# Optimization experiments

Hardware: AMD Instinct MI355X
Metric: run time of the kernel (lower is better)

Reference implementation:

```python
import jax, jax.numpy as jnp
import numpy as np

B, S, D, H, FF = 4, 2048, 1024, 16, 4096
HD = D // H


def setup_inputs() -> dict:
    key = jax.random.key(0)
    ks = jax.random.split(key, 12)
    s = 1.0 / np.sqrt(D)
    sf = 1.0 / np.sqrt(FF)
    return {
        "x": jax.random.normal(ks[0], (B, S, D), dtype=jnp.float32),
        "lengths": jax.random.randint(ks[1], (B,), 1, S + 1, dtype=jnp.int32),
        "qW": jax.random.uniform(ks[2], (D, D), jnp.float32, -s, s),
        "qb": jnp.zeros((D,), jnp.float32),
        "kW": jax.random.uniform(ks[3], (D, D), jnp.float32, -s, s),
        "kb": jnp.zeros((D,), jnp.float32),
        "vW": jax.random.uniform(ks[4], (D, D), jnp.float32, -s, s),
        "vb": jnp.zeros((D,), jnp.float32),
        "oW": jax.random.uniform(ks[5], (D, D), jnp.float32, -s, s),
        "ob": jnp.zeros((D,), jnp.float32),
        "w1": jax.random.uniform(ks[6], (D, FF), jnp.float32, -s, s),
        "b1": jnp.zeros((FF,), jnp.float32),
        "w2": jax.random.uniform(ks[7], (FF, D), jnp.float32, -sf, sf),
        "b2": jnp.zeros((D,), jnp.float32),
    }


def _heads(t):
    # [B,S,D] -> [B,H,S,HD]
    return t.reshape(B, S, H, HD).transpose(0, 2, 1, 3)


def reference(x, lengths, qW, qb, kW, kb, vW, vb, oW, ob, w1, b1, w2, b2):
    q = _heads(x @ qW + qb)
    k = _heads(x @ kW + kb)
    v = _heads(x @ vW + vb)
    scale = 1.0 / np.sqrt(HD)
    logits = jnp.einsum("bhqd,bhkd->bhqk", q, k) * scale  # [B,H,S,S]
    # key-position mask: pos >= length -> -inf
    mask = jnp.arange(S)[None, None, None, :] >= lengths[:, None, None, None]
    logits = jnp.where(mask, -jnp.inf, logits)
    a = jax.nn.softmax(logits, axis=-1)
    ctx = jnp.einsum("bhqk,bhkd->bhqd", a, v)
    ctx = ctx.transpose(0, 2, 1, 3).reshape(B, S, D)
    attn_out = ctx @ oW + ob
    h = jax.nn.relu(attn_out @ w1 + b1)
    return h @ w2 + b2
```

## Files before the change

### kernel.cpp

```cpp
#include <hip/hip_runtime.h>


typedef short bf16x8 __attribute__((ext_vector_type(8)));
typedef float f32x4 __attribute__((ext_vector_type(4)));

__device__ __forceinline__ unsigned short f2bf(float f) {
  unsigned int u = __builtin_bit_cast(unsigned int, f);
  u += 0x7fffu + ((u >> 16) & 1u);
  return (unsigned short)(u >> 16);
}

__device__ __forceinline__ void gload16(const unsigned short* g, unsigned short* l) {
  __builtin_amdgcn_global_load_lds(
      (const __attribute__((address_space(1))) unsigned int*)(g),
      (__attribute__((address_space(3))) unsigned int*)(l),
      16, 0, 0);
}

__global__ __launch_bounds__(256) void cast_f32_bf16(
    const float* __restrict__ src, unsigned short* __restrict__ dst, int n4) {
  int i = blockIdx.x * 256 + threadIdx.x;
  if (i < n4) {
    float4 f = ((const float4*)src)[i];
    ushort4 o;
    o.x = f2bf(f.x); o.y = f2bf(f.y); o.z = f2bf(f.z); o.w = f2bf(f.w);
    ((ushort4*)dst)[i] = o;
  }
}

__global__ __launch_bounds__(256) void prep_weights(
    const float* __restrict__ qW, const float* __restrict__ kW,
    const float* __restrict__ vW, const float* __restrict__ oW,
    const float* __restrict__ w1, const float* __restrict__ w2,
    unsigned short* __restrict__ qWt, unsigned short* __restrict__ kWt,
    unsigned short* __restrict__ vWt, unsigned short* __restrict__ oWt,
    unsigned short* __restrict__ w1t, unsigned short* __restrict__ w2t) {
  const int t = blockIdx.x;
  const float* W; unsigned short* Wt; int N, K, nt, kt;
  if (t < 2048) {
    const int w = t >> 9, r = t & 511;
    nt = r & 15; kt = r >> 4; N = 1024; K = 1024;
    W  = w == 0 ? qW : w == 1 ? kW : w == 2 ? vW : oW;
    Wt = w == 0 ? qWt : w == 1 ? kWt : w == 2 ? vWt : oWt;
  } else if (t < 4096) {
    const int r = t - 2048;
    nt = r & 63; kt = r >> 6; N = 4096; K = 1024; W = w1; Wt = w1t;
  } else {
    const int r = t - 4096;
    nt = r & 15; kt = r >> 4; N = 1024; K = 4096; W = w2; Wt = w2t;
  }
  const int wave = threadIdx.x >> 6, lane = threadIdx.x & 63;
  const int n = nt * 64 + lane;
  const int k0 = kt * 32 + wave * 8;
  union { int4 v; unsigned short u[8]; } s;
#pragma unroll
  for (int j = 0; j < 8; ++j) s.u[j] = f2bf(W[(size_t)(k0 + j) * N + n]);
  *(int4*)(Wt + (size_t)n * K + k0) = s.v;
}

template <int EPI>
__global__ __launch_bounds__(256) void gemm_bt(
    const unsigned short* __restrict__ A, const unsigned short* __restrict__ Bt,
    const float* __restrict__ bias, void* __restrict__ C,
    int M, int N, int K) {
  __shared__ unsigned short As[128 * 32];
  __shared__ unsigned short Bs[128 * 32];

  const int tid = threadIdx.x;
  const int wave = tid >> 6, lane = tid & 63;
  const int quad = lane >> 4, l16 = lane & 15;
  const int wm = (wave >> 1) * 64, wn = (wave & 1) * 64;

  const int NT = N >> 7, band = NT >> 3;
  const int xcd = blockIdx.x & 7, local = blockIdx.x >> 3;
  const int nt = xcd * band + local % band;
  const int mt = local / band;
  const int m0 = mt * 128, n0 = nt * 128;

  const int u1 = tid, u2 = 256 + tid;
  const int r1 = u1 >> 2, c1 = (u1 & 3) * 8;
  const int r2 = u2 >> 2, c2 = (u2 & 3) * 8;
  const unsigned short* ga1 = A + (size_t)(m0 + r1) * K + c1;
  const unsigned short* ga2 = A + (size_t)(m0 + r2) * K + c2;
  const unsigned short* gb1 = Bt + (size_t)(n0 + r1) * K + c1;
  const unsigned short* gb2 = Bt + (size_t)(n0 + r2) * K + c2;
  unsigned short* lA1 = As + wave * 512;
  unsigned short* lA2 = As + 2048 + wave * 512;
  unsigned short* lB1 = Bs + wave * 512;
  unsigned short* lB2 = Bs + 2048 + wave * 512;

  f32x4 acc[4][4] = {};

  for (int k0 = 0; k0 < K; k0 += 32) {
    __syncthreads();
    gload16(ga1 + k0, lA1);
    gload16(ga2 + k0, lA2);
    gload16(gb1 + k0, lB1);
    gload16(gb2 + k0, lB2);
    __syncthreads();

    bf16x8 af[4], bfr[4];
#pragma unroll
    for (int mi = 0; mi < 4; ++mi)
      af[mi] = *(const bf16x8*)(As + (wm + mi * 16 + l16) * 32 + quad * 8);
#pragma unroll
    for (int ni = 0; ni < 4; ++ni)
      bfr[ni] = *(const bf16x8*)(Bs + (wn + ni * 16 + l16) * 32 + quad * 8);
#pragma unroll
    for (int mi = 0; mi < 4; ++mi)
#pragma unroll
      for (int ni = 0; ni < 4; ++ni)
        acc[mi][ni] = __builtin_amdgcn_mfma_f32_16x16x32_bf16(
            af[mi], bfr[ni], acc[mi][ni], 0, 0, 0);
  }

#pragma unroll
  for (int ni = 0; ni < 4; ++ni) {
    const int col = n0 + wn + ni * 16 + l16;
    const float bv = bias[col];
#pragma unroll
    for (int mi = 0; mi < 4; ++mi) {
      const int row = m0 + wm + mi * 16 + quad * 4;
#pragma unroll
      for (int r = 0; r < 4; ++r) {
        float v = acc[mi][ni][r] + bv;
        if (EPI == 2) v = v > 0.f ? v : 0.f;
        if (EPI == 0)
          ((float*)C)[(size_t)(row + r) * N + col] = v;
        else
          ((unsigned short*)C)[(size_t)(row + r) * N + col] = f2bf(v);
      }
    }
  }
}

#define QSCALE 0.180336884f

__global__ __launch_bounds__(256) void gemm_qkv(
    const unsigned short* __restrict__ A, const unsigned short* __restrict__ Bt,
    const float* __restrict__ qb, const float* __restrict__ kb,
    const float* __restrict__ vb, unsigned short* __restrict__ Qo,
    unsigned short* __restrict__ Ko, unsigned short* __restrict__ Vto,
    int M, int K) {
  __shared__ unsigned short As[128 * 32];
  __shared__ unsigned short Bs[128 * 32];

  const int tid = threadIdx.x;
  const int wave = tid >> 6, lane = tid & 63;
  const int quad = lane >> 4, l16 = lane & 15;
  const int wm = (wave >> 1) * 64, wn = (wave & 1) * 64;

  const int NT = 24, band = 3;
  const int xcd = blockIdx.x & 7, local = blockIdx.x >> 3;
  const int nt = xcd * band + local % band;
  const int mt = local / band;
  const int m0 = mt * 128, n0 = nt * 128;

  const int u1 = tid, u2 = 256 + tid;
  const int r1 = u1 >> 2, c1 = (u1 & 3) * 8;
  const int r2 = u2 >> 2, c2 = (u2 & 3) * 8;
  const unsigned short* ga1 = A + (size_t)(m0 + r1) * K + c1;
  const unsigned short* ga2 = A + (size_t)(m0 + r2) * K + c2;
  const unsigned short* gb1 = Bt + (size_t)(n0 + r1) * K + c1;
  const unsigned short* gb2 = Bt + (size_t)(n0 + r2) * K + c2;
  unsigned short* lA1 = As + wave * 512;
  unsigned short* lA2 = As + 2048 + wave * 512;
  unsigned short* lB1 = Bs + wave * 512;
  unsigned short* lB2 = Bs + 2048 + wave * 512;

  f32x4 acc[4][4] = {};

  for (int k0 = 0; k0 < K; k0 += 32) {
    __syncthreads();
    gload16(ga1 + k0, lA1);
    gload16(ga2 + k0, lA2);
    gload16(gb1 + k0, lB1);
    gload16(gb2 + k0, lB2);
    __syncthreads();

    bf16x8 af[4], bfr[4];
#pragma unroll
    for (int mi = 0; mi < 4; ++mi)
      af[mi] = *(const bf16x8*)(As + (wm + mi * 16 + l16) * 32 + quad * 8);
#pragma unroll
    for (int ni = 0; ni < 4; ++ni)
      bfr[ni] = *(const bf16x8*)(Bs + (wn + ni * 16 + l16) * 32 + quad * 8);
#pragma unroll
    for (int mi = 0; mi < 4; ++mi)
#pragma unroll
      for (int ni = 0; ni < 4; ++ni)
        acc[mi][ni] = __builtin_amdgcn_mfma_f32_16x16x32_bf16(
            af[mi], bfr[ni], acc[mi][ni], 0, 0, 0);
  }

  const int seg = n0 >> 10;
  const float* bias = seg == 0 ? qb : (seg == 1 ? kb : vb);
#pragma unroll
  for (int ni = 0; ni < 4; ++ni) {
    const int col = (n0 + wn + ni * 16 + l16) & 1023;
    const float bv = bias[col];
#pragma unroll
    for (int mi = 0; mi < 4; ++mi) {
      const int row = m0 + wm + mi * 16 + quad * 4;
      if (seg == 2) {
        const int b = row >> 11, s = row & 2047;
        const int h = col >> 6, dh = col & 63;
        union { ushort4 v; unsigned short u[4]; } pk;
#pragma unroll
        for (int r = 0; r < 4; ++r) pk.u[r] = f2bf(acc[mi][ni][r] + bv);
        *(ushort4*)(Vto + ((size_t)((b * 16 + h) * 64 + dh)) * 2048 + s) = pk.v;
      } else {
#pragma unroll
        for (int r = 0; r < 4; ++r) {
          float v = acc[mi][ni][r] + bv;
          if (seg == 0)
            Qo[(size_t)(row + r) * 1024 + col] = f2bf(v * QSCALE);
          else
            Ko[(size_t)(row + r) * 1024 + col] = f2bf(v);
        }
      }
    }
  }
}

__global__ __launch_bounds__(256, 4) void attn_fused(
    const unsigned short* __restrict__ Q, const unsigned short* __restrict__ K,
    const unsigned short* __restrict__ Vt, const int* __restrict__ lengths,
    unsigned short* __restrict__ ctx) {
  constexpr int S = 2048, D = 1024;
  __shared__ unsigned short Ks[64 * 72];
  __shared__ unsigned short Vs[64 * 72];
  __shared__ unsigned short Ps[4 * 32 * 72];

  const int tid = threadIdx.x;
  const int wave = tid >> 6, lane = tid & 63;
  const int quad = lane >> 4, l16 = lane & 15;
  const int bid = blockIdx.x;
  const int qt = bid & 15;
  const int h = (bid >> 4) & 15;
  const int b = bid >> 8;
  const int q0 = qt * 128;
  const int len = lengths[b];
  const int ktEnd = (len + 63) >> 6;
  const float NEGINF = -__builtin_inff();

  const size_t xbase = (size_t)b * S * D + (size_t)h * 64;
  const size_t vtb = (size_t)(b * 16 + h) * 64;

  bf16x8 qf0[2], qf1[2];
#pragma unroll
  for (int mb = 0; mb < 2; ++mb) {
    const unsigned short* qrow =
        Q + xbase + (size_t)(q0 + wave * 32 + mb * 16 + l16) * D;
    qf0[mb] = *(const bf16x8*)(qrow + quad * 8);
    qf1[mb] = *(const bf16x8*)(qrow + 32 + quad * 8);
  }

  const int sr1 = tid >> 3, sc1 = (tid & 7) * 8;
  const int sr2 = (256 + tid) >> 3, sc2 = (tid & 7) * 8;
  const unsigned short* kg1 = K + xbase + (size_t)sr1 * D + sc1;
  const unsigned short* kg2 = K + xbase + (size_t)sr2 * D + sc2;
  const unsigned short* vg1 = Vt + (vtb + sr1) * S + sc1;
  const unsigned short* vg2 = Vt + (vtb + sr2) * S + sc2;

  f32x4 oacc[2][4] = {};
  float rs[2][4] = {};

  unsigned short* pw = Ps + wave * (32 * 72);

  for (int kt = 0; kt < ktEnd; ++kt) {
    const int k0 = kt * 64;
    __syncthreads();
    *(int4*)(Ks + sr1 * 72 + sc1) = *(const int4*)(kg1 + (size_t)k0 * D);
    *(int4*)(Ks + sr2 * 72 + sc2) = *(const int4*)(kg2 + (size_t)k0 * D);
    *(int4*)(Vs + sr1 * 72 + sc1) = *(const int4*)(vg1 + k0);
    *(int4*)(Vs + sr2 * 72 + sc2) = *(const int4*)(vg2 + k0);
    __syncthreads();

    f32x4 sf[2][4];
#pragma unroll
    for (int cb = 0; cb < 4; ++cb) {
      const bf16x8 kf0 = *(const bf16x8*)(Ks + (cb * 16 + l16) * 72 + quad * 8);
      const bf16x8 kf1 = *(const bf16x8*)(Ks + (cb * 16 + l16) * 72 + 32 + quad * 8);
#pragma unroll
      for (int mb = 0; mb < 2; ++mb) {
        f32x4 c = {0.f, 0.f, 0.f, 0.f};
        c = __builtin_amdgcn_mfma_f32_16x16x32_bf16(qf0[mb], kf0, c, 0, 0, 0);
        c = __builtin_amdgcn_mfma_f32_16x16x32_bf16(qf1[mb], kf1, c, 0, 0, 0);
        sf[mb][cb] = c;
      }
    }

    if (k0 + 64 > len) {
#pragma unroll
      for (int cb = 0; cb < 4; ++cb) {
        const bool msk = (k0 + cb * 16 + l16) >= len;
#pragma unroll
        for (int mb = 0; mb < 2; ++mb)
#pragma unroll
          for (int r = 0; r < 4; ++r) sf[mb][cb][r] = msk ? NEGINF : sf[mb][cb][r];
      }
    }

#pragma unroll
    for (int mb = 0; mb < 2; ++mb)
#pragma unroll
      for (int cb = 0; cb < 4; ++cb)
#pragma unroll
        for (int r = 0; r < 4; ++r) {
          const float p = __builtin_amdgcn_exp2f(sf[mb][cb][r]);
          sf[mb][cb][r] = p;
          rs[mb][r] += p;
        }

#pragma unroll
    for (int mb = 0; mb < 2; ++mb)
#pragma unroll
      for (int cb = 0; cb < 4; ++cb)
#pragma unroll
        for (int r = 0; r < 4; ++r)
          pw[(mb * 16 + quad * 4 + r) * 72 + cb * 16 + l16] = f2bf(sf[mb][cb][r]);

    bf16x8 pa0[2], pa1[2];
#pragma unroll
    for (int mb = 0; mb < 2; ++mb) {
      pa0[mb] = *(const bf16x8*)(pw + (mb * 16 + l16) * 72 + quad * 8);
      pa1[mb] = *(const bf16x8*)(pw + (mb * 16 + l16) * 72 + 32 + quad * 8);
    }
#pragma unroll
    for (int cb = 0; cb < 4; ++cb) {
      const bf16x8 vb0 = *(const bf16x8*)(Vs + (cb * 16 + l16) * 72 + quad * 8);
      const bf16x8 vb1 = *(const bf16x8*)(Vs + (cb * 16 + l16) * 72 + 32 + quad * 8);
#pragma unroll
      for (int mb = 0; mb < 2; ++mb) {
        oacc[mb][cb] = __builtin_amdgcn_mfma_f32_16x16x32_bf16(pa0[mb], vb0, oacc[mb][cb], 0, 0, 0);
        oacc[mb][cb] = __builtin_amdgcn_mfma_f32_16x16x32_bf16(pa1[mb], vb1, oacc[mb][cb], 0, 0, 0);
      }
    }
  }

#pragma unroll
  for (int off = 8; off > 0; off >>= 1)
#pragma unroll
    for (int mb = 0; mb < 2; ++mb)
#pragma unroll
      for (int r = 0; r < 4; ++r) rs[mb][r] += __shfl_xor(rs[mb][r], off, 16);

#pragma unroll
  for (int mb = 0; mb < 2; ++mb) {
    float inv[4];
#pragma unroll
    for (int r = 0; r < 4; ++r) inv[r] = 1.0f / rs[mb][r];
#pragma unroll
    for (int cb = 0; cb < 4; ++cb)
#pragma unroll
      for (int r = 0; r < 4; ++r) {
        const int row = q0 + wave * 32 + mb * 16 + quad * 4 + r;
        ctx[xbase + (size_t)row * D + cb * 16 + l16] = f2bf(oacc[mb][cb][r] * inv[r]);
      }
  }
}

extern "C" void kernel_launch(void* const* d_in, const int* in_sizes, int n_in,
                              void* d_out, int out_size, void* d_ws,
                              size_t ws_size, hipStream_t stream) {
  const float* x  = (const float*)d_in[0];
  const int* lengths = (const int*)d_in[1];
  const float* qW = (const float*)d_in[2];
  const float* qb = (const float*)d_in[3];
  const float* kW = (const float*)d_in[4];
  const float* kb = (const float*)d_in[5];
  const float* vW = (const float*)d_in[6];
  const float* vb = (const float*)d_in[7];
  const float* oW = (const float*)d_in[8];
  const float* ob = (const float*)d_in[9];
  const float* w1 = (const float*)d_in[10];
  const float* b1 = (const float*)d_in[11];
  const float* w2 = (const float*)d_in[12];
  const float* b2 = (const float*)d_in[13];
  float* out = (float*)d_out;

  const int Bx = 4, S = 2048, D = 1024, FF = 4096;
  const int M = Bx * S;

  unsigned short* p = (unsigned short*)d_ws;
  unsigned short* xb  = p; p += (size_t)M * D;
  unsigned short* qWt = p; p += (size_t)D * D;
  unsigned short* kWt = p; p += (size_t)D * D;
  unsigned short* vWt = p; p += (size_t)D * D;
  unsigned short* oWt = p; p += (size_t)D * D;
  unsigned short* w1t = p; p += (size_t)D * FF;
  unsigned short* w2t = p; p += (size_t)FF * D;
  unsigned short* Qb  = p; p += (size_t)M * D;
  unsigned short* Kb  = p; p += (size_t)M * D;
  unsigned short* Vtb = p; p += (size_t)M * D;
  unsigned short* Cb  = p; p += (size_t)M * D;
  unsigned short* Ab  = p; p += (size_t)M * D;
  unsigned short* Hb  = p; p += (size_t)M * FF;

  {
    int n4 = (int)((size_t)M * D / 4);
    cast_f32_bf16<<<dim3((n4 + 255) / 256), dim3(256), 0, stream>>>(x, xb, n4);
  }
  prep_weights<<<dim3(6144), dim3(256), 0, stream>>>(
      qW, kW, vW, oW, w1, w2, qWt, kWt, vWt, oWt, w1t, w2t);

  dim3 blk(256);
  gemm_qkv<<<dim3((3 * D / 128) * (M / 128)), blk, 0, stream>>>(
      xb, qWt, qb, kb, vb, Qb, Kb, Vtb, M, D);

  attn_fused<<<dim3(Bx * 16 * (S / 128)), blk, 0, stream>>>(Qb, Kb, Vtb, lengths, Cb);

  gemm_bt<1><<<dim3((D / 128) * (M / 128)), blk, 0, stream>>>(Cb, oWt, ob, Ab, M, D, D);
  gemm_bt<2><<<dim3((FF / 128) * (M / 128)), blk, 0, stream>>>(Ab, w1t, b1, Hb, M, FF, D);
  gemm_bt<0><<<dim3((D / 128) * (M / 128)), blk, 0, stream>>>(Hb, w2t, b2, out, M, D, FF);
}
```

Measured before the change: 509.4 us.

## Use 256x256-tile, 4-stage pipelined GEMM for QKV and FFN1 projections

Adds a 512-thread GEMM core with 256x256 output tiles, a 4-buffer async global-to-LDS pipeline using vmcnt waits, XOR-swizzled LDS layout and MFMA priority raising. The QKV projection and the first FFN GEMM switch to it, while the o-projection and FFN2 keep the old 128-tile kernel. The aim is to cut global traffic per flop, hide load latency and avoid LDS bank conflicts. In exchange it uses 128KB of LDS and one block per CU, which leaves fewer blocks than CUs (384 and 512 tiles).

```diff
diff --git a/kernel.cpp b/kernel.cpp
--- a/kernel.cpp
+++ b/kernel.cpp
@@ -58,6 +58,168 @@
   *(int4*)(Wt + (size_t)n * K + k0) = s.v;
 }
 
+__device__ __forceinline__ void gemm256_core(
+    const unsigned short* __restrict__ A, const unsigned short* __restrict__ Bt,
+    unsigned short* __restrict__ As, unsigned short* __restrict__ Bs,
+    const int m0, const int n0, const int K, f32x4 (&acc)[8][4]) {
+  const int tid = (int)threadIdx.x;
+  const int w = tid >> 6, l = tid & 63;
+  const int quad = l >> 4, l16 = l & 15;
+  const int wm = (w >> 2) * 128, wn = (w & 3) * 64;
+
+  const int lr = l >> 2, lc = l & 3;
+  const int swz = (lc ^ ((l >> 3) & 3)) * 8;
+  const unsigned short* gA[2]; const unsigned short* gB[2];
+  unsigned short* dA[2]; unsigned short* dB[2];
+#pragma unroll
+  for (int j = 0; j < 2; ++j) {
+    const int rr = (w * 2 + j) * 16 + lr;
+    gA[j] = A + (size_t)(m0 + rr) * K + swz;
+    gB[j] = Bt + (size_t)(n0 + rr) * K + swz;
+    dA[j] = As + (w * 2 + j) * 512;
+    dB[j] = Bs + (w * 2 + j) * 512;
+  }
+
+  const int cread = (quad ^ ((l16 >> 1) & 3)) * 8;
+  const int rA = (wm + l16) * 32;
+  const int rB = (wn + l16) * 32;
+
+  auto STAGE = [&](int db, int t) {
+#pragma unroll
+    for (int j = 0; j < 2; ++j) {
+      gload16(gA[j] + t * 32, dA[j] + db * 8192);
+      gload16(gB[j] + t * 32, dB[j] + db * 8192);
+    }
+  };
+  auto COMPUTE = [&](int db) {
+    bf16x8 af[8], bf[4];
+    const unsigned short* pa = As + db * 8192 + rA + cread;
+    const unsigned short* pb = Bs + db * 8192 + rB + cread;
+#pragma unroll
+    for (int ni = 0; ni < 4; ++ni) bf[ni] = *(const bf16x8*)(pb + ni * 16 * 32);
+#pragma unroll
+    for (int mi = 0; mi < 8; ++mi) af[mi] = *(const bf16x8*)(pa + mi * 16 * 32);
+    __builtin_amdgcn_s_setprio(1);
+#pragma unroll
+    for (int mi = 0; mi < 8; ++mi)
+#pragma unroll
+      for (int ni = 0; ni < 4; ++ni)
+        acc[mi][ni] = __builtin_amdgcn_mfma_f32_16x16x32_bf16(
+            af[mi], bf[ni], acc[mi][ni], 0, 0, 0);
+    __builtin_amdgcn_s_setprio(0);
+  };
+
+  const int NK = K >> 5;
+  STAGE(0, 0); STAGE(1, 1); STAGE(2, 2);
+#pragma unroll 1
+  for (int t = 0; t < NK - 3; ++t) {
+    asm volatile("s_waitcnt vmcnt(8)" ::: "memory");
+    __builtin_amdgcn_s_barrier();
+    STAGE((t + 3) & 3, t + 3);
+    COMPUTE(t & 3);
+  }
+  asm volatile("s_waitcnt vmcnt(8)" ::: "memory");
+  __builtin_amdgcn_s_barrier();
+  COMPUTE((NK - 3) & 3);
+  asm volatile("s_waitcnt vmcnt(4)" ::: "memory");
+  __builtin_amdgcn_s_barrier();
+  COMPUTE((NK - 2) & 3);
+  asm volatile("s_waitcnt vmcnt(0)" ::: "memory");
+  __builtin_amdgcn_s_barrier();
+  COMPUTE((NK - 1) & 3);
+}
+
+template <int EPI>
+__global__ __launch_bounds__(512, 1) void gemm256_bt(
+    const unsigned short* __restrict__ A, const unsigned short* __restrict__ Bt,
+    const float* __restrict__ bias, void* __restrict__ C, int N, int K) {
+  __shared__ unsigned short As[4 * 8192];
+  __shared__ unsigned short Bs[4 * 8192];
+  const int tn = N >> 8;
+  const int cpx = (int)gridDim.x >> 3;
+  const int sw = ((int)blockIdx.x & 7) * cpx + ((int)blockIdx.x >> 3);
+  const int nt = sw % tn, mt = sw / tn;
+  const int m0 = mt * 256, n0 = nt * 256;
+
+  f32x4 acc[8][4] = {};
+  gemm256_core(A, Bt, As, Bs, m0, n0, K, acc);
+
+  const int tid = (int)threadIdx.x;
+  const int w = tid >> 6, l = tid & 63;
+  const int quad = l >> 4, l16 = l & 15;
+  const int wm = (w >> 2) * 128, wn = (w & 3) * 64;
+#pragma unroll
+  for (int ni = 0; ni < 4; ++ni) {
+    const int col = n0 + wn + ni * 16 + l16;
+    const float bv = bias[col];
+#pragma unroll
+    for (int mi = 0; mi < 8; ++mi) {
+      const int row = m0 + wm + mi * 16 + quad * 4;
+#pragma unroll
+      for (int r = 0; r < 4; ++r) {
+        float v = acc[mi][ni][r] + bv;
+        if (EPI == 2) v = v > 0.f ? v : 0.f;
+        if (EPI == 0)
+          ((float*)C)[(size_t)(row + r) * N + col] = v;
+        else
+          ((unsigned short*)C)[(size_t)(row + r) * N + col] = f2bf(v);
+      }
+    }
+  }
+}
+
+#define QSCALE 0.180336884f
+
+__global__ __launch_bounds__(512, 1) void gemm256_qkv(
+    const unsigned short* __restrict__ A, const unsigned short* __restrict__ Bt,
+    const float* __restrict__ qb, const float* __restrict__ kb,
+    const float* __restrict__ vb, unsigned short* __restrict__ Qo,
+    unsigned short* __restrict__ Ko, unsigned short* __restrict__ Vto, int K) {
+  __shared__ unsigned short As[4 * 8192];
+  __shared__ unsigned short Bs[4 * 8192];
+  const int tn = 12;
+  const int cpx = (int)gridDim.x >> 3;
+  const int sw = ((int)blockIdx.x & 7) * cpx + ((int)blockIdx.x >> 3);
+  const int nt = sw % tn, mt = sw / tn;
+  const int m0 = mt * 256, n0 = nt * 256;
+
+  f32x4 acc[8][4] = {};
+  gemm256_core(A, Bt, As, Bs, m0, n0, K, acc);
+
+  const int tid = (int)threadIdx.x;
+  const int w = tid >> 6, l = tid & 63;
+  const int quad = l >> 4, l16 = l & 15;
+  const int wm = (w >> 2) * 128, wn = (w & 3) * 64;
+
+  const int seg = n0 >> 10;
+  const float* bias = seg == 0 ? qb : (seg == 1 ? kb : vb);
+#pragma unroll
+  for (int ni = 0; ni < 4; ++ni) {
+    const int col = (n0 + wn + ni * 16 + l16) & 1023;
+    const float bv = bias[col];
+#pragma unroll
+    for (int mi = 0; mi < 8; ++mi) {
+      const int row = m0 + wm + mi * 16 + quad * 4;
+      if (seg == 2) {
+        const int b = row >> 11, s = row & 2047;
+        const int hh = col >> 6, dh = col & 63;
+        union { ushort4 v; unsigned short u[4]; } pk;
+#pragma unroll
+        for (int r = 0; r < 4; ++r) pk.u[r] = f2bf(acc[mi][ni][r] + bv);
+        *(ushort4*)(Vto + ((size_t)((b * 16 + hh) * 64 + dh)) * 2048 + s) = pk.v;
+      } else if (seg == 0) {
+#pragma unroll
+        for (int r = 0; r < 4; ++r)
+          Qo[(size_t)(row + r) * 1024 + col] = f2bf((acc[mi][ni][r] + bv) * QSCALE);
+      } else {
+#pragma unroll
+        for (int r = 0; r < 4; ++r)
+          Ko[(size_t)(row + r) * 1024 + col] = f2bf(acc[mi][ni][r] + bv);
+      }
+    }
+  }
+}
+
 template <int EPI>
 __global__ __launch_bounds__(256) void gemm_bt(
     const unsigned short* __restrict__ A, const unsigned short* __restrict__ Bt,
@@ -129,95 +291,6 @@
           ((float*)C)[(size_t)(row + r) * N + col] = v;
         else
           ((unsigned short*)C)[(size_t)(row + r) * N + col] = f2bf(v);
-      }
-    }
-  }
-}
-
-#define QSCALE 0.180336884f
-
-__global__ __launch_bounds__(256) void gemm_qkv(
-    const unsigned short* __restrict__ A, const unsigned short* __restrict__ Bt,
-    const float* __restrict__ qb, const float* __restrict__ kb,
-    const float* __restrict__ vb, unsigned short* __restrict__ Qo,
-    unsigned short* __restrict__ Ko, unsigned short* __restrict__ Vto,
-    int M, int K) {
-  __shared__ unsigned short As[128 * 32];
-  __shared__ unsigned short Bs[128 * 32];
-
-  const int tid = threadIdx.x;
-  const int wave = tid >> 6, lane = tid & 63;
-  const int quad = lane >> 4, l16 = lane & 15;
-  const int wm = (wave >> 1) * 64, wn = (wave & 1) * 64;
-
-  const int NT = 24, band = 3;
-  const int xcd = blockIdx.x & 7, local = blockIdx.x >> 3;
-  const int nt = xcd * band + local % band;
-  const int mt = local / band;
-  const int m0 = mt * 128, n0 = nt * 128;
-
-  const int u1 = tid, u2 = 256 + tid;
-  const int r1 = u1 >> 2, c1 = (u1 & 3) * 8;
-  const int r2 = u2 >> 2, c2 = (u2 & 3) * 8;
-  const unsigned short* ga1 = A + (size_t)(m0 + r1) * K + c1;
-  const unsigned short* ga2 = A + (size_t)(m0 + r2) * K + c2;
-  const unsigned short* gb1 = Bt + (size_t)(n0 + r1) * K + c1;
-  const unsigned short* gb2 = Bt + (size_t)(n0 + r2) * K + c2;
-  unsigned short* lA1 = As + wave * 512;
-  unsigned short* lA2 = As + 2048 + wave * 512;
-  unsigned short* lB1 = Bs + wave * 512;
-  unsigned short* lB2 = Bs + 2048 + wave * 512;
-
-  f32x4 acc[4][4] = {};
-
-  for (int k0 = 0; k0 < K; k0 += 32) {
-    __syncthreads();
-    gload16(ga1 + k0, lA1);
-    gload16(ga2 + k0, lA2);
-    gload16(gb1 + k0, lB1);
-    gload16(gb2 + k0, lB2);
-    __syncthreads();
-
-    bf16x8 af[4], bfr[4];
-#pragma unroll
-    for (int mi = 0; mi < 4; ++mi)
-      af[mi] = *(const bf16x8*)(As + (wm + mi * 16 + l16) * 32 + quad * 8);
-#pragma unroll
-    for (int ni = 0; ni < 4; ++ni)
-      bfr[ni] = *(const bf16x8*)(Bs + (wn + ni * 16 + l16) * 32 + quad * 8);
-#pragma unroll
-    for (int mi = 0; mi < 4; ++mi)
-#pragma unroll
-      for (int ni = 0; ni < 4; ++ni)
-        acc[mi][ni] = __builtin_amdgcn_mfma_f32_16x16x32_bf16(
-            af[mi], bfr[ni], acc[mi][ni], 0, 0, 0);
-  }
-
-  const int seg = n0 >> 10;
-  const float* bias = seg == 0 ? qb : (seg == 1 ? kb : vb);
-#pragma unroll
-  for (int ni = 0; ni < 4; ++ni) {
-    const int col = (n0 + wn + ni * 16 + l16) & 1023;
-    const float bv = bias[col];
-#pragma unroll
-    for (int mi = 0; mi < 4; ++mi) {
-      const int row = m0 + wm + mi * 16 + quad * 4;
-      if (seg == 2) {
-        const int b = row >> 11, s = row & 2047;
-        const int h = col >> 6, dh = col & 63;
-        union { ushort4 v; unsigned short u[4]; } pk;
-#pragma unroll
-        for (int r = 0; r < 4; ++r) pk.u[r] = f2bf(acc[mi][ni][r] + bv);
-        *(ushort4*)(Vto + ((size_t)((b * 16 + h) * 64 + dh)) * 2048 + s) = pk.v;
-      } else {
-#pragma unroll
-        for (int r = 0; r < 4; ++r) {
-          float v = acc[mi][ni][r] + bv;
-          if (seg == 0)
-            Qo[(size_t)(row + r) * 1024 + col] = f2bf(v * QSCALE);
-          else
-            Ko[(size_t)(row + r) * 1024 + col] = f2bf(v);
-        }
       }
     }
   }
@@ -405,13 +478,15 @@
   prep_weights<<<dim3(6144), dim3(256), 0, stream>>>(
       qW, kW, vW, oW, w1, w2, qWt, kWt, vWt, oWt, w1t, w2t);
 
-  dim3 blk(256);
-  gemm_qkv<<<dim3((3 * D / 128) * (M / 128)), blk, 0, stream>>>(
-      xb, qWt, qb, kb, vb, Qb, Kb, Vtb, M, D);
-
-  attn_fused<<<dim3(Bx * 16 * (S / 128)), blk, 0, stream>>>(Qb, Kb, Vtb, lengths, Cb);
-
-  gemm_bt<1><<<dim3((D / 128) * (M / 128)), blk, 0, stream>>>(Cb, oWt, ob, Ab, M, D, D);
-  gemm_bt<2><<<dim3((FF / 128) * (M / 128)), blk, 0, stream>>>(Ab, w1t, b1, Hb, M, FF, D);
-  gemm_bt<0><<<dim3((D / 128) * (M / 128)), blk, 0, stream>>>(Hb, w2t, b2, out, M, D, FF);
-}
+  gemm256_qkv<<<dim3(384), dim3(512), 0, stream>>>(
+      xb, qWt, qb, kb, vb, Qb, Kb, Vtb, D);
+
+  attn_fused<<<dim3(Bx * 16 * (S / 128)), dim3(256), 0, stream>>>(
+      Qb, Kb, Vtb, lengths, Cb);
+
+  gemm_bt<1><<<dim3((D / 128) * (M / 128)), dim3(256), 0, stream>>>(
+      Cb, oWt, ob, Ab, M, D, D);
+  gemm256_bt<2><<<dim3(512), dim3(512), 0, stream>>>(Ab, w1t, b1, Hb, FF, D);
+  gemm_bt<0><<<dim3((D / 128) * (M / 128)), dim3(256), 0, stream>>>(
+      Hb, w2t, b2, out, M, D, FF);
+}
```

Result: slower. 529.0 us (+3.8%).
